# Kernel optimization log

Measured on AMD Instinct MI355X. Metric: run time of the kernel, lower is better.

## Reference

```python
import jax, jax.numpy as jnp
import numpy as np

N_NODES = 50000
N_EDGES = 1600000
D_IN = 128
D_OUT = 32
ALPHA = 0.2  # LeakyReLU negative slope


def setup_inputs() -> dict:
    key = jax.random.key(0)
    k1, k2, k3, k4, k5, k6 = jax.random.split(key, 6)
    gain = float(np.sqrt(2.0))  # relu gain, xavier_normal-style scale
    X = jax.random.normal(k1, (N_NODES, D_IN), dtype=jnp.float32)
    weights = jax.random.normal(k2, (D_IN, D_OUT), dtype=jnp.float32) * (gain * np.sqrt(2.0 / (D_IN + D_OUT)))
    a0 = jax.random.normal(k3, (1, D_OUT), dtype=jnp.float32) * (gain * np.sqrt(2.0 / (1 + D_OUT)))
    a1 = jax.random.normal(k4, (1, D_OUT), dtype=jnp.float32) * (gain * np.sqrt(2.0 / (1 + D_OUT)))
    row_idx = jax.random.randint(k5, (N_EDGES,), 0, N_NODES, dtype=jnp.int32)
    col_idx = jax.random.randint(k6, (N_EDGES,), 0, N_NODES, dtype=jnp.int32)
    return {"X": X, "weights": weights, "a0": a0, "a1": a1,
            "row_idx": row_idx, "col_idx": col_idx}


def _minmax_norm(v):
    vmin = jnp.min(v)
    vmax = jnp.max(v)
    return (v - vmin) / (vmax - vmin)


def reference(X, weights, a0, a1, row_idx, col_idx):
    # X_prime = X @ W  -> [N, D]
    X_prime = X @ weights
    # Per-node partial scores; edge score e(i->j) = a0.X_prime[i] + a1.X_prime[j]
    s0 = jnp.sum(X_prime * a0, axis=-1)  # [N]
    s1 = jnp.sum(X_prime * a1, axis=-1)  # [N]
    att = s0[row_idx] + s1[col_idx]      # [E]
    # leakyrelu -> min-max normalize over all edges -> exp
    att = jax.nn.leaky_relu(att, negative_slope=ALPHA)
    att = jnp.exp(_minmax_norm(att))
    # rows_sum = SpMM(att, ones) = per-destination-row sum of edge weights
    rows_sum = jax.ops.segment_sum(att, row_idx, num_segments=N_NODES)  # [N]
    # h_prime = SpMM(att, X_prime) / rows_sum  (dropout p=0 -> identity)
    h = jax.ops.segment_sum(att[:, None] * X_prime[col_idx], row_idx,
                            num_segments=N_NODES)  # [N, D]
    return h / rows_sum[:, None]
```

## Files before the change

kernel.cpp:

```cpp
#include <hip/hip_runtime.h>
#include <hip/hip_bf16.h>
#include <math.h>

#define N_NODES 50000
#define N_EDGES 1600000
#define D_IN 128
#define D_OUT 32
#define ALPHA 0.2f

#define NB   1021
#define NBP  1024
#define RPB  49
#define CAP  2048
#define PT   8
#define PBK  256
#define EB   (PT * PBK)
#define NPB  ((N_EDGES + EB - 1) / EB)
#define XNPB 32
#define NXB  ((N_NODES + XNPB - 1) / XNPB)
#define XLS  33

__device__ __forceinline__ int enc_f(float x) {
    int i = __float_as_int(x);
    return i >= 0 ? i : (i ^ 0x7fffffff);
}
__device__ __forceinline__ float dec_f(int k) {
    return __int_as_float(k >= 0 ? k : (k ^ 0x7fffffff));
}
__device__ __forceinline__ unsigned short f2bf(float x) {
    __hip_bfloat16 h = __float2bfloat16(x);
    return *(unsigned short*)&h;
}
__device__ __forceinline__ float bf2f(unsigned short u) {
    return __uint_as_float((unsigned)u << 16);
}

__global__ __launch_bounds__(256) void k_gemm(const float* __restrict__ X,
                                              const float* __restrict__ W,
                                              const float* __restrict__ a0,
                                              const float* __restrict__ a1,
                                              unsigned short* __restrict__ Xpb,
                                              float* __restrict__ s0,
                                              float* __restrict__ s1,
                                              int* __restrict__ minmax,
                                              int* __restrict__ gcount) {
    __shared__ float4 Wl4[1024];
    __shared__ float4 Xl4[XNPB * XLS];
    const int tid = threadIdx.x;
    if (blockIdx.x == 0) {
        if (tid == 0) {
            minmax[0] = 0x7fffffff;
            minmax[1] = (int)0x80000000;
        }
        for (int i = tid; i < NBP; i += 256) gcount[i] = 0;
    }
    const int node0 = blockIdx.x * XNPB;
    {
        const float4* W4 = (const float4*)W;
#pragma unroll
        for (int i = 0; i < 4; ++i) Wl4[tid + 256 * i] = W4[tid + 256 * i];
        const float4* X4 = (const float4*)X + (size_t)node0 * (D_IN / 4);
        const int lim = (min(XNPB, N_NODES - node0)) * (D_IN / 4);
#pragma unroll
        for (int i = 0; i < 4; ++i) {
            const int idx = tid + 256 * i;
            const float4 v = (idx < lim) ? X4[idx]
                                         : make_float4(0.f, 0.f, 0.f, 0.f);
            Xl4[(idx >> 5) * XLS + (idx & 31)] = v;
        }
    }
    __syncthreads();
    const int g = tid >> 3;
    const int l = tid & 7;
    const int node = node0 + g;
    const float4* xr = &Xl4[g * XLS];
    float ax = 0.f, ay = 0.f, az = 0.f, aw = 0.f;
#pragma unroll 4
    for (int kk = 0; kk < D_IN / 4; ++kk) {
        const float4 xv = xr[kk];
        const float4 w0 = Wl4[(4 * kk + 0) * 8 + l];
        const float4 w1 = Wl4[(4 * kk + 1) * 8 + l];
        const float4 w2 = Wl4[(4 * kk + 2) * 8 + l];
        const float4 w3 = Wl4[(4 * kk + 3) * 8 + l];
        ax += xv.x * w0.x + xv.y * w1.x + xv.z * w2.x + xv.w * w3.x;
        ay += xv.x * w0.y + xv.y * w1.y + xv.z * w2.y + xv.w * w3.y;
        az += xv.x * w0.z + xv.y * w1.z + xv.z * w2.z + xv.w * w3.z;
        aw += xv.x * w0.w + xv.y * w1.w + xv.z * w2.w + xv.w * w3.w;
    }
    if (node < N_NODES) {
        uint2 pk;
        pk.x = ((unsigned)f2bf(ay) << 16) | f2bf(ax);
        pk.y = ((unsigned)f2bf(aw) << 16) | f2bf(az);
        ((uint2*)Xpb)[(size_t)node * 8 + l] = pk;
        const float4 av0 = ((const float4*)a0)[l];
        const float4 av1 = ((const float4*)a1)[l];
        float v0 = ax * av0.x + ay * av0.y + az * av0.z + aw * av0.w;
        float v1 = ax * av1.x + ay * av1.y + az * av1.z + aw * av1.w;
#pragma unroll
        for (int m = 4; m >= 1; m >>= 1) {
            v0 += __shfl_xor(v0, m);
            v1 += __shfl_xor(v1, m);
        }
        if (l == 0) { s0[node] = v0; s1[node] = v1; }
    }
}

__global__ __launch_bounds__(256) void k_edge(const int* __restrict__ row,
                                              const int* __restrict__ col,
                                              const float* __restrict__ s0,
                                              const float* __restrict__ s1,
                                              int* __restrict__ minmax,
                                              int* __restrict__ gcount,
                                              uint2* __restrict__ gEdges) {
    __shared__ int hist[NBP];
    __shared__ int lcur[NBP];
    __shared__ int smn[4], smx[4];
    const int tid = threadIdx.x;
    for (int i = tid; i < NBP; i += PBK) hist[i] = 0;
    __syncthreads();
    const int base = blockIdx.x * EB;
    unsigned px[PT];
    float    fa[PT];
    int cnt = 0;
    int kmin = 0x7fffffff, kmax = 0x80000000;
    if (base + EB <= N_EDGES) {
#pragma unroll
        for (int i = 0; i < PT / 4; ++i) {
            const int4 r4 = ((const int4*)(row + base))[tid + i * PBK];
            const int4 c4 = ((const int4*)(col + base))[tid + i * PBK];
            const int rr[4] = {r4.x, r4.y, r4.z, r4.w};
            const int cc[4] = {c4.x, c4.y, c4.z, c4.w};
#pragma unroll
            for (int j = 0; j < 4; ++j) {
                const int r = rr[j];
                const int c = cc[j];
                float a = s0[r] + s1[c];
                a = a > 0.f ? a : ALPHA * a;
                const int k = enc_f(a);
                kmin = min(kmin, k);
                kmax = max(kmax, k);
                const unsigned b = (unsigned)r / RPB;
                const unsigned lr = (unsigned)r - b * RPB;
                px[cnt] = (b << 22) | (lr << 16) | (unsigned)c;
                fa[cnt] = a;
                ++cnt;
                atomicAdd(&hist[b], 1);
            }
        }
    } else {
#pragma unroll
        for (int i = 0; i < PT; ++i) {
            const int e = base + i * PBK + tid;
            if (e >= N_EDGES) break;
            const int r = row[e];
            const int c = col[e];
            float a = s0[r] + s1[c];
            a = a > 0.f ? a : ALPHA * a;
            const int k = enc_f(a);
            kmin = min(kmin, k);
            kmax = max(kmax, k);
            const unsigned b = (unsigned)r / RPB;
            const unsigned lr = (unsigned)r - b * RPB;
            px[cnt] = (b << 22) | (lr << 16) | (unsigned)c;
            fa[cnt] = a;
            ++cnt;
            atomicAdd(&hist[b], 1);
        }
    }
    __syncthreads();
    for (int i = tid; i < NBP; i += PBK) {
        const int h = hist[i];
        lcur[i] = h > 0 ? atomicAdd(&gcount[i], h) : 0;
    }
    __syncthreads();
    for (int j = 0; j < cnt; ++j) {
        const unsigned p = px[j];
        const unsigned b = p >> 22;
        const int pos = atomicAdd(&lcur[b], 1);
        if (pos < CAP)
            gEdges[(size_t)b * CAP + pos] =
                make_uint2(p & 0x3FFFFFu, (unsigned)__float_as_int(fa[j]));
    }
#pragma unroll
    for (int m = 32; m >= 1; m >>= 1) {
        kmin = min(kmin, __shfl_xor(kmin, m));
        kmax = max(kmax, __shfl_xor(kmax, m));
    }
    const int wave = tid >> 6;
    if ((tid & 63) == 0) { smn[wave] = kmin; smx[wave] = kmax; }
    __syncthreads();
    if (tid == 0) {
#pragma unroll
        for (int w = 1; w < 4; ++w) {
            kmin = min(kmin, smn[w]);
            kmax = max(kmax, smx[w]);
        }
        atomicMin(&minmax[0], kmin);
        atomicMax(&minmax[1], kmax);
    }
}

__global__ __launch_bounds__(512, 8) void k_bucket(const int* __restrict__ gcount,
                                                   const uint2* __restrict__ gEdges,
                                                   const unsigned short* __restrict__ Xpb,
                                                   const int* __restrict__ minmax,
                                                   float* __restrict__ out) {
    __shared__ unsigned short scol[CAP];
    __shared__ float swt[CAP];
    __shared__ int off[RPB + 1];
    __shared__ int cur[RPB];
    const int b = blockIdx.x;
    const int t = threadIdx.x;
    const float mn = dec_f(minmax[0]);
    const float mx = dec_f(minmax[1]);
    const float inv = 1.0f / (mx - mn);
    const int cnt = min(gcount[b], CAP);
    const uint2* eb = gEdges + (size_t)b * CAP;

    if (t < RPB) cur[t] = 0;
    __syncthreads();
    for (int i = t; i < cnt; i += 512) atomicAdd(&cur[eb[i].x >> 16], 1);
    __syncthreads();
    if (t == 0) {
        int run = 0;
#pragma unroll
        for (int r = 0; r < RPB; ++r) { off[r] = run; run += cur[r]; }
        off[RPB] = run;
    }
    __syncthreads();
    if (t < RPB) cur[t] = off[t];
    __syncthreads();
    for (int i = t; i < cnt; i += 512) {
        const uint2 e = eb[i];
        const int lr = (int)(e.x >> 16);
        const int p = atomicAdd(&cur[lr], 1);
        if (p < CAP) {
            scol[p] = (unsigned short)(e.x & 0xFFFFu);
            swt[p] = __expf((__int_as_float(e.y) - mn) * inv);
        }
    }
    __syncthreads();

    const int proc = t >> 4;
    const int d2 = t & 15;
    const unsigned* Xp32 = (const unsigned*)Xpb;
    for (int lr = proc; lr < RPB; lr += 32) {
        const int s = off[lr];
        const int e2 = off[lr + 1];
        float pa0 = 0.f, pa1 = 0.f, pa2 = 0.f, pa3 = 0.f;
        float pb0 = 0.f, pb1 = 0.f, pb2 = 0.f, pb3 = 0.f;
        float w0s = 0.f, w1s = 0.f, w2s = 0.f, w3s = 0.f;
        int i = s;
        for (; i + 3 < e2; i += 4) {
            const int c0 = scol[i];
            const int c1 = scol[i + 1];
            const int c2 = scol[i + 2];
            const int c3 = scol[i + 3];
            const float w0 = swt[i];
            const float w1 = swt[i + 1];
            const float w2 = swt[i + 2];
            const float w3 = swt[i + 3];
            const unsigned u0 = Xp32[(size_t)c0 * 16 + d2];
            const unsigned u1 = Xp32[(size_t)c1 * 16 + d2];
            const unsigned u2 = Xp32[(size_t)c2 * 16 + d2];
            const unsigned u3 = Xp32[(size_t)c3 * 16 + d2];
            pa0 += w0 * bf2f((unsigned short)(u0 & 0xFFFFu));
            pb0 += w0 * bf2f((unsigned short)(u0 >> 16));
            pa1 += w1 * bf2f((unsigned short)(u1 & 0xFFFFu));
            pb1 += w1 * bf2f((unsigned short)(u1 >> 16));
            pa2 += w2 * bf2f((unsigned short)(u2 & 0xFFFFu));
            pb2 += w2 * bf2f((unsigned short)(u2 >> 16));
            pa3 += w3 * bf2f((unsigned short)(u3 & 0xFFFFu));
            pb3 += w3 * bf2f((unsigned short)(u3 >> 16));
            w0s += w0; w1s += w1; w2s += w2; w3s += w3;
        }
        for (; i < e2; ++i) {
            const float w = swt[i];
            const unsigned u = Xp32[(size_t)scol[i] * 16 + d2];
            pa0 += w * bf2f((unsigned short)(u & 0xFFFFu));
            pb0 += w * bf2f((unsigned short)(u >> 16));
            w0s += w;
        }
        const int r = b * RPB + lr;
        if (r < N_NODES) {
            const float ws = w0s + w1s + w2s + w3s;
            float2 o;
            o.x = (pa0 + pa1 + pa2 + pa3) / ws;
            o.y = (pb0 + pb1 + pb2 + pb3) / ws;
            ((float2*)out)[(size_t)r * 16 + d2] = o;
        }
    }
}

extern "C" void kernel_launch(void* const* d_in, const int* in_sizes, int n_in,
                              void* d_out, int out_size, void* d_ws, size_t ws_size,
                              hipStream_t stream) {
    const float* X  = (const float*)d_in[0];
    const float* W  = (const float*)d_in[1];
    const float* a0 = (const float*)d_in[2];
    const float* a1 = (const float*)d_in[3];
    const int* row  = (const int*)d_in[4];
    const int* col  = (const int*)d_in[5];
    float* out = (float*)d_out;

    float* ws = (float*)d_ws;
    int*   minmax = (int*)ws;
    int*   gcount = (int*)(ws + 64);
    float* s0 = ws + 64 + 2048;
    float* s1 = s0 + 50048;
    unsigned short* Xpb = (unsigned short*)(s1 + 50048);
    uint2* gEdges = (uint2*)(s1 + 50048 + 800000);

    k_gemm<<<NXB, 256, 0, stream>>>(X, W, a0, a1, Xpb, s0, s1, minmax, gcount);
    k_edge<<<NPB, 256, 0, stream>>>(row, col, s0, s1, minmax, gcount, gEdges);
    k_bucket<<<NB, 512, 0, stream>>>(gcount, gEdges, Xpb, minmax, out);
}
```

Measured before the change: 158.4 us.

## Decouple score computation via W·a and overlap GEMM with edge binning

A new lightweight kernel folds the attention vectors into the weights first (W·a0, W·a1), so the per-node scores come from a single dot product against X and no longer depend on the full X@W GEMM. The bf16 X' GEMM then runs in the same launch as the edge scoring and binning pass, with blocks interleaved 2:1, so the compute-heavy and atomic-heavy work can overlap. Per-bucket global counters are padded to a 16-int stride to cut atomic contention on shared cache lines. The cost is reading X twice and changing the floating-point summation order of the scores.

Measured after the change: 156.6 us. Within noise of the previous version (-1.1%).

```diff
diff --git a/kernel.cpp b/kernel.cpp
--- a/kernel.cpp
+++ b/kernel.cpp
@@ -12,6 +12,7 @@
 #define NBP  1024
 #define RPB  49
 #define CAP  2048
+#define GST  16
 #define PT   8
 #define PBK  256
 #define EB   (PT * PBK)
@@ -19,6 +20,7 @@
 #define XNPB 32
 #define NXB  ((N_NODES + XNPB - 1) / XNPB)
 #define XLS  33
+#define SNPB 32
 
 __device__ __forceinline__ int enc_f(float x) {
     int i = __float_as_int(x);
@@ -35,67 +37,54 @@
     return __uint_as_float((unsigned)u << 16);
 }
 
-__global__ __launch_bounds__(256) void k_gemm(const float* __restrict__ X,
-                                              const float* __restrict__ W,
-                                              const float* __restrict__ a0,
-                                              const float* __restrict__ a1,
-                                              unsigned short* __restrict__ Xpb,
-                                              float* __restrict__ s0,
-                                              float* __restrict__ s1,
-                                              int* __restrict__ minmax,
-                                              int* __restrict__ gcount) {
-    __shared__ float4 Wl4[1024];
-    __shared__ float4 Xl4[XNPB * XLS];
+__global__ __launch_bounds__(256) void k_s(const float* __restrict__ X,
+                                           const float* __restrict__ W,
+                                           const float* __restrict__ a0,
+                                           const float* __restrict__ a1,
+                                           float* __restrict__ s0,
+                                           float* __restrict__ s1,
+                                           int* __restrict__ minmax,
+                                           int* __restrict__ gcount) {
+    __shared__ float wa0[D_IN], wa1[D_IN];
     const int tid = threadIdx.x;
     if (blockIdx.x == 0) {
         if (tid == 0) {
             minmax[0] = 0x7fffffff;
             minmax[1] = (int)0x80000000;
         }
-        for (int i = tid; i < NBP; i += 256) gcount[i] = 0;
-    }
-    const int node0 = blockIdx.x * XNPB;
+        int4* g4 = (int4*)gcount;
+        for (int i = tid; i < NBP * GST / 4; i += 256)
+            g4[i] = make_int4(0, 0, 0, 0);
+    }
     {
-        const float4* W4 = (const float4*)W;
-#pragma unroll
-        for (int i = 0; i < 4; ++i) Wl4[tid + 256 * i] = W4[tid + 256 * i];
-        const float4* X4 = (const float4*)X + (size_t)node0 * (D_IN / 4);
-        const int lim = (min(XNPB, N_NODES - node0)) * (D_IN / 4);
-#pragma unroll
-        for (int i = 0; i < 4; ++i) {
-            const int idx = tid + 256 * i;
-            const float4 v = (idx < lim) ? X4[idx]
-                                         : make_float4(0.f, 0.f, 0.f, 0.f);
-            Xl4[(idx >> 5) * XLS + (idx & 31)] = v;
-        }
-    }
-    __syncthreads();
-    const int g = tid >> 3;
+        const int k = tid & 127;
+        const float4* Wr = (const float4*)(W + k * D_OUT);
+        const float4* A = (const float4*)((tid < 128) ? a0 : a1);
+        float acc = 0.f;
+#pragma unroll
+        for (int j = 0; j < 8; ++j) {
+            const float4 w = Wr[j];
+            const float4 a = A[j];
+            acc += w.x * a.x + w.y * a.y + w.z * a.z + w.w * a.w;
+        }
+        if (tid < 128) wa0[k] = acc; else wa1[k] = acc;
+    }
+    __syncthreads();
+    const int node = blockIdx.x * SNPB + (tid >> 3);
     const int l = tid & 7;
-    const int node = node0 + g;
-    const float4* xr = &Xl4[g * XLS];
-    float ax = 0.f, ay = 0.f, az = 0.f, aw = 0.f;
-#pragma unroll 4
-    for (int kk = 0; kk < D_IN / 4; ++kk) {
-        const float4 xv = xr[kk];
-        const float4 w0 = Wl4[(4 * kk + 0) * 8 + l];
-        const float4 w1 = Wl4[(4 * kk + 1) * 8 + l];
-        const float4 w2 = Wl4[(4 * kk + 2) * 8 + l];
-        const float4 w3 = Wl4[(4 * kk + 3) * 8 + l];
-        ax += xv.x * w0.x + xv.y * w1.x + xv.z * w2.x + xv.w * w3.x;
-        ay += xv.x * w0.y + xv.y * w1.y + xv.z * w2.y + xv.w * w3.y;
-        az += xv.x * w0.z + xv.y * w1.z + xv.z * w2.z + xv.w * w3.z;
-        aw += xv.x * w0.w + xv.y * w1.w + xv.z * w2.w + xv.w * w3.w;
-    }
     if (node < N_NODES) {
-        uint2 pk;
-        pk.x = ((unsigned)f2bf(ay) << 16) | f2bf(ax);
-        pk.y = ((unsigned)f2bf(aw) << 16) | f2bf(az);
-        ((uint2*)Xpb)[(size_t)node * 8 + l] = pk;
-        const float4 av0 = ((const float4*)a0)[l];
-        const float4 av1 = ((const float4*)a1)[l];
-        float v0 = ax * av0.x + ay * av0.y + az * av0.z + aw * av0.w;
-        float v1 = ax * av1.x + ay * av1.y + az * av1.z + aw * av1.w;
+        const float4* xr = (const float4*)(X + (size_t)node * D_IN) + l * 4;
+        const float4* p4 = (const float4*)wa0 + l * 4;
+        const float4* q4 = (const float4*)wa1 + l * 4;
+        float v0 = 0.f, v1 = 0.f;
+#pragma unroll
+        for (int j = 0; j < 4; ++j) {
+            const float4 x = xr[j];
+            const float4 p = p4[j];
+            const float4 q = q4[j];
+            v0 += x.x * p.x + x.y * p.y + x.z * p.z + x.w * p.w;
+            v1 += x.x * q.x + x.y * q.y + x.z * q.z + x.w * q.w;
+        }
 #pragma unroll
         for (int m = 4; m >= 1; m >>= 1) {
             v0 += __shfl_xor(v0, m);
@@ -105,35 +94,108 @@
     }
 }
 
-__global__ __launch_bounds__(256) void k_edge(const int* __restrict__ row,
-                                              const int* __restrict__ col,
-                                              const float* __restrict__ s0,
-                                              const float* __restrict__ s1,
-                                              int* __restrict__ minmax,
-                                              int* __restrict__ gcount,
-                                              uint2* __restrict__ gEdges) {
-    __shared__ int hist[NBP];
-    __shared__ int lcur[NBP];
-    __shared__ int smn[4], smx[4];
+__global__ __launch_bounds__(256) void k_fused(const float* __restrict__ X,
+                                               const float* __restrict__ W,
+                                               const int* __restrict__ row,
+                                               const int* __restrict__ col,
+                                               const float* __restrict__ s0,
+                                               const float* __restrict__ s1,
+                                               unsigned short* __restrict__ Xpb,
+                                               int* __restrict__ minmax,
+                                               int* __restrict__ gcount,
+                                               uint2* __restrict__ gEdges) {
+    __shared__ char smem[33280] __attribute__((aligned(16)));
     const int tid = threadIdx.x;
-    for (int i = tid; i < NBP; i += PBK) hist[i] = 0;
-    __syncthreads();
-    const int base = blockIdx.x * EB;
-    unsigned px[PT];
-    float    fa[PT];
-    int cnt = 0;
-    int kmin = 0x7fffffff, kmax = 0x80000000;
-    if (base + EB <= N_EDGES) {
-#pragma unroll
-        for (int i = 0; i < PT / 4; ++i) {
-            const int4 r4 = ((const int4*)(row + base))[tid + i * PBK];
-            const int4 c4 = ((const int4*)(col + base))[tid + i * PBK];
-            const int rr[4] = {r4.x, r4.y, r4.z, r4.w};
-            const int cc[4] = {c4.x, c4.y, c4.z, c4.w};
-#pragma unroll
-            for (int j = 0; j < 4; ++j) {
-                const int r = rr[j];
-                const int c = cc[j];
+    const int bid = blockIdx.x;
+    if (bid % 3 != 0) {
+        const int gid = bid - bid / 3 - 1;
+        if (gid >= NXB) return;
+        float4* Wl4 = (float4*)smem;
+        float4* Xl4 = (float4*)(smem + 16384);
+        const int node0 = gid * XNPB;
+        {
+            const float4* W4 = (const float4*)W;
+#pragma unroll
+            for (int i = 0; i < 4; ++i) Wl4[tid + 256 * i] = W4[tid + 256 * i];
+            const float4* X4 = (const float4*)X + (size_t)node0 * (D_IN / 4);
+            const int lim = (min(XNPB, N_NODES - node0)) * (D_IN / 4);
+#pragma unroll
+            for (int i = 0; i < 4; ++i) {
+                const int idx = tid + 256 * i;
+                const float4 v = (idx < lim) ? X4[idx]
+                                             : make_float4(0.f, 0.f, 0.f, 0.f);
+                Xl4[(idx >> 5) * XLS + (idx & 31)] = v;
+            }
+        }
+        __syncthreads();
+        const int g = tid >> 3;
+        const int l = tid & 7;
+        const int node = node0 + g;
+        const float4* xr = &Xl4[g * XLS];
+        float ax = 0.f, ay = 0.f, az = 0.f, aw = 0.f;
+#pragma unroll 4
+        for (int kk = 0; kk < D_IN / 4; ++kk) {
+            const float4 xv = xr[kk];
+            const float4 w0 = Wl4[(4 * kk + 0) * 8 + l];
+            const float4 w1 = Wl4[(4 * kk + 1) * 8 + l];
+            const float4 w2 = Wl4[(4 * kk + 2) * 8 + l];
+            const float4 w3 = Wl4[(4 * kk + 3) * 8 + l];
+            ax += xv.x * w0.x + xv.y * w1.x + xv.z * w2.x + xv.w * w3.x;
+            ay += xv.x * w0.y + xv.y * w1.y + xv.z * w2.y + xv.w * w3.y;
+            az += xv.x * w0.z + xv.y * w1.z + xv.z * w2.z + xv.w * w3.z;
+            aw += xv.x * w0.w + xv.y * w1.w + xv.z * w2.w + xv.w * w3.w;
+        }
+        if (node < N_NODES) {
+            uint2 pk;
+            pk.x = ((unsigned)f2bf(ay) << 16) | f2bf(ax);
+            pk.y = ((unsigned)f2bf(aw) << 16) | f2bf(az);
+            ((uint2*)Xpb)[(size_t)node * 8 + l] = pk;
+        }
+    } else {
+        const int bb = bid / 3;
+        if (bb >= NPB) return;
+        int* hist = (int*)smem;
+        int* lcur = (int*)(smem + 4096);
+        int* smn  = (int*)(smem + 8192);
+        int* smx  = (int*)(smem + 8256);
+        for (int i = tid; i < NBP; i += PBK) hist[i] = 0;
+        __syncthreads();
+        const int base = bb * EB;
+        unsigned px[PT];
+        float    fa[PT];
+        int cnt = 0;
+        int kmin = 0x7fffffff, kmax = 0x80000000;
+        if (base + EB <= N_EDGES) {
+#pragma unroll
+            for (int i = 0; i < PT / 4; ++i) {
+                const int4 r4 = ((const int4*)(row + base))[tid + i * PBK];
+                const int4 c4 = ((const int4*)(col + base))[tid + i * PBK];
+                const int rr[4] = {r4.x, r4.y, r4.z, r4.w};
+                const int cc[4] = {c4.x, c4.y, c4.z, c4.w};
+#pragma unroll
+                for (int j = 0; j < 4; ++j) {
+                    const int r = rr[j];
+                    const int c = cc[j];
+                    float a = s0[r] + s1[c];
+                    a = a > 0.f ? a : ALPHA * a;
+                    const int k = enc_f(a);
+                    kmin = min(kmin, k);
+                    kmax = max(kmax, k);
+                    const unsigned b = (unsigned)r / RPB;
+                    const unsigned lr = (unsigned)r - b * RPB;
+                    px[cnt] = (b << 22) | (lr << 16) | (unsigned)c;
+                    fa[cnt] = a;
+                    ++cnt;
+                    atomicAdd(&hist[b], 1);
+                }
+            }
+        } else {
+#pragma unroll
+            for (int i = 0; i < PT; ++i) {
+                const int e = base + i * PBK + tid;
+                if (e >= N_EDGES) break;
+                const int r = row[e];
+                const int c = col[e];
                 float a = s0[r] + s1[c];
                 a = a > 0.f ? a : ALPHA * a;
                 const int k = enc_f(a);
@@ -147,56 +209,37 @@
                 atomicAdd(&hist[b], 1);
             }
         }
-    } else {
-#pragma unroll
-        for (int i = 0; i < PT; ++i) {
-            const int e = base + i * PBK + tid;
-            if (e >= N_EDGES) break;
-            const int r = row[e];
-            const int c = col[e];
-            float a = s0[r] + s1[c];
-            a = a > 0.f ? a : ALPHA * a;
-            const int k = enc_f(a);
-            kmin = min(kmin, k);
-            kmax = max(kmax, k);
-            const unsigned b = (unsigned)r / RPB;
-            const unsigned lr = (unsigned)r - b * RPB;
-            px[cnt] = (b << 22) | (lr << 16) | (unsigned)c;
-            fa[cnt] = a;
-            ++cnt;
-            atomicAdd(&hist[b], 1);
-        }
-    }
-    __syncthreads();
-    for (int i = tid; i < NBP; i += PBK) {
-        const int h = hist[i];
-        lcur[i] = h > 0 ? atomicAdd(&gcount[i], h) : 0;
-    }
-    __syncthreads();
-    for (int j = 0; j < cnt; ++j) {
-        const unsigned p = px[j];
-        const unsigned b = p >> 22;
-        const int pos = atomicAdd(&lcur[b], 1);
-        if (pos < CAP)
-            gEdges[(size_t)b * CAP + pos] =
-                make_uint2(p & 0x3FFFFFu, (unsigned)__float_as_int(fa[j]));
-    }
-#pragma unroll
-    for (int m = 32; m >= 1; m >>= 1) {
-        kmin = min(kmin, __shfl_xor(kmin, m));
-        kmax = max(kmax, __shfl_xor(kmax, m));
-    }
-    const int wave = tid >> 6;
-    if ((tid & 63) == 0) { smn[wave] = kmin; smx[wave] = kmax; }
-    __syncthreads();
-    if (tid == 0) {
-#pragma unroll
-        for (int w = 1; w < 4; ++w) {
-            kmin = min(kmin, smn[w]);
-            kmax = max(kmax, smx[w]);
-        }
-        atomicMin(&minmax[0], kmin);
-        atomicMax(&minmax[1], kmax);
+        __syncthreads();
+        for (int i = tid; i < NBP; i += PBK) {
+            const int h = hist[i];
+            lcur[i] = h > 0 ? atomicAdd(&gcount[i << 4], h) : 0;
+        }
+        __syncthreads();
+        for (int j = 0; j < cnt; ++j) {
+            const unsigned p = px[j];
+            const unsigned b = p >> 22;
+            const int pos = atomicAdd(&lcur[b], 1);
+            if (pos < CAP)
+                gEdges[(size_t)b * CAP + pos] =
+                    make_uint2(p & 0x3FFFFFu, (unsigned)__float_as_int(fa[j]));
+        }
+#pragma unroll
+        for (int m = 32; m >= 1; m >>= 1) {
+            kmin = min(kmin, __shfl_xor(kmin, m));
+            kmax = max(kmax, __shfl_xor(kmax, m));
+        }
+        const int wave = tid >> 6;
+        if ((tid & 63) == 0) { smn[wave] = kmin; smx[wave] = kmax; }
+        __syncthreads();
+        if (tid == 0) {
+#pragma unroll
+            for (int w = 1; w < 4; ++w) {
+                kmin = min(kmin, smn[w]);
+                kmax = max(kmax, smx[w]);
+            }
+            atomicMin(&minmax[0], kmin);
+            atomicMax(&minmax[1], kmax);
+        }
     }
 }
 
@@ -214,7 +257,7 @@
     const float mn = dec_f(minmax[0]);
     const float mx = dec_f(minmax[1]);
     const float inv = 1.0f / (mx - mn);
-    const int cnt = min(gcount[b], CAP);
+    const int cnt = min(gcount[b << 4], CAP);
     const uint2* eb = gEdges + (size_t)b * CAP;
 
     if (t < RPB) cur[t] = 0;
@@ -306,12 +349,14 @@
     float* ws = (float*)d_ws;
     int*   minmax = (int*)ws;
     int*   gcount = (int*)(ws + 64);
-    float* s0 = ws + 64 + 2048;
+    float* s0 = ws + 64 + NBP * GST;
     float* s1 = s0 + 50048;
     unsigned short* Xpb = (unsigned short*)(s1 + 50048);
     uint2* gEdges = (uint2*)(s1 + 50048 + 800000);
 
-    k_gemm<<<NXB, 256, 0, stream>>>(X, W, a0, a1, Xpb, s0, s1, minmax, gcount);
-    k_edge<<<NPB, 256, 0, stream>>>(row, col, s0, s1, minmax, gcount, gEdges);
+    k_s<<<(N_NODES + SNPB - 1) / SNPB, 256, 0, stream>>>(X, W, a0, a1, s0, s1,
+                                                         minmax, gcount);
+    k_fused<<<NXB + NPB + 1, 256, 0, stream>>>(X, W, row, col, s0, s1, Xpb,
+                                               minmax, gcount, gEdges);
     k_bucket<<<NB, 512, 0, stream>>>(gcount, gEdges, Xpb, minmax, out);
 }
```

## Replace LDS histogram binning with padded global atomics and per-block minmax partials

Applied to the files above, without the earlier changes.

The edge kernel drops its shared-memory histogram and two-pass local cursor scheme. Each edge now claims its slot with a direct global atomicAdd on a bucket counter padded to 16 ints (one per 64-byte line) and is written immediately. Blocks shrink to 4 edges per thread, and the global atomicMin/Max is replaced by per-block min/max partials. Every bucket block re-reduces those partials, trading 1.6M global atomics and some redundant reduction work for fewer barriers, smaller register state and higher occupancy.

Result: slower. 192.0 us (+21.2%).

```diff
diff --git a/kernel.cpp b/kernel.cpp
--- a/kernel.cpp
+++ b/kernel.cpp
@@ -12,10 +12,11 @@
 #define NBP  1024
 #define RPB  49
 #define CAP  2048
-#define PT   8
-#define PBK  256
-#define EB   (PT * PBK)
-#define NPB  ((N_EDGES + EB - 1) / EB)
+#define GST  16
+#define EPT  4
+#define EBK  256
+#define EB   (EPT * EBK)
+#define NEB  ((N_EDGES + EB - 1) / EB)
 #define XNPB 32
 #define NXB  ((N_NODES + XNPB - 1) / XNPB)
 #define XLS  33
@@ -42,17 +43,15 @@
                                               unsigned short* __restrict__ Xpb,
                                               float* __restrict__ s0,
                                               float* __restrict__ s1,
-                                              int* __restrict__ minmax,
                                               int* __restrict__ gcount) {
     __shared__ float4 Wl4[1024];
     __shared__ float4 Xl4[XNPB * XLS];
     const int tid = threadIdx.x;
     if (blockIdx.x == 0) {
-        if (tid == 0) {
-            minmax[0] = 0x7fffffff;
-            minmax[1] = (int)0x80000000;
-        }
-        for (int i = tid; i < NBP; i += 256) gcount[i] = 0;
+        int4* g4 = (int4*)gcount;
+#pragma unroll
+        for (int i = 0; i < NBP * GST / 4 / 256; ++i)
+            g4[tid + 256 * i] = make_int4(0, 0, 0, 0);
     }
     const int node0 = blockIdx.x * XNPB;
     {
@@ -109,77 +108,59 @@
                                               const int* __restrict__ col,
                                               const float* __restrict__ s0,
                                               const float* __restrict__ s1,
-                                              int* __restrict__ minmax,
                                               int* __restrict__ gcount,
+                                              int2* __restrict__ mm,
                                               uint2* __restrict__ gEdges) {
-    __shared__ int hist[NBP];
-    __shared__ int lcur[NBP];
     __shared__ int smn[4], smx[4];
     const int tid = threadIdx.x;
-    for (int i = tid; i < NBP; i += PBK) hist[i] = 0;
-    __syncthreads();
     const int base = blockIdx.x * EB;
-    unsigned px[PT];
-    float    fa[PT];
-    int cnt = 0;
     int kmin = 0x7fffffff, kmax = 0x80000000;
     if (base + EB <= N_EDGES) {
-#pragma unroll
-        for (int i = 0; i < PT / 4; ++i) {
-            const int4 r4 = ((const int4*)(row + base))[tid + i * PBK];
-            const int4 c4 = ((const int4*)(col + base))[tid + i * PBK];
-            const int rr[4] = {r4.x, r4.y, r4.z, r4.w};
-            const int cc[4] = {c4.x, c4.y, c4.z, c4.w};
-#pragma unroll
-            for (int j = 0; j < 4; ++j) {
-                const int r = rr[j];
-                const int c = cc[j];
-                float a = s0[r] + s1[c];
+        const int4 r4 = ((const int4*)(row + base))[tid];
+        const int4 c4 = ((const int4*)(col + base))[tid];
+        const int rr[4] = {r4.x, r4.y, r4.z, r4.w};
+        const int cc[4] = {c4.x, c4.y, c4.z, c4.w};
+        float sr[4], sc[4];
+#pragma unroll
+        for (int j = 0; j < 4; ++j) { sr[j] = s0[rr[j]]; sc[j] = s1[cc[j]]; }
+#pragma unroll
+        for (int j = 0; j < 4; ++j) {
+            float a = sr[j] + sc[j];
+            a = a > 0.f ? a : ALPHA * a;
+            const int k = enc_f(a);
+            kmin = min(kmin, k);
+            kmax = max(kmax, k);
+            const unsigned r = (unsigned)rr[j];
+            const unsigned b = r / RPB;
+            const unsigned lr = r - b * RPB;
+            const int pos = atomicAdd(&gcount[b << 4], 1);
+            if (pos < CAP)
+                gEdges[(size_t)b * CAP + pos] =
+                    make_uint2((lr << 16) | (unsigned)cc[j],
+                               (unsigned)__float_as_int(a));
+        }
+    } else {
+#pragma unroll
+        for (int j = 0; j < 4; ++j) {
+            const int e = base + j * EBK + tid;
+            if (e < N_EDGES) {
+                const int rv = row[e];
+                const int cv = col[e];
+                float a = s0[rv] + s1[cv];
                 a = a > 0.f ? a : ALPHA * a;
                 const int k = enc_f(a);
                 kmin = min(kmin, k);
                 kmax = max(kmax, k);
-                const unsigned b = (unsigned)r / RPB;
-                const unsigned lr = (unsigned)r - b * RPB;
-                px[cnt] = (b << 22) | (lr << 16) | (unsigned)c;
-                fa[cnt] = a;
-                ++cnt;
-                atomicAdd(&hist[b], 1);
+                const unsigned r = (unsigned)rv;
+                const unsigned b = r / RPB;
+                const unsigned lr = r - b * RPB;
+                const int pos = atomicAdd(&gcount[b << 4], 1);
+                if (pos < CAP)
+                    gEdges[(size_t)b * CAP + pos] =
+                        make_uint2((lr << 16) | (unsigned)cv,
+                                   (unsigned)__float_as_int(a));
             }
         }
-    } else {
-#pragma unroll
-        for (int i = 0; i < PT; ++i) {
-            const int e = base + i * PBK + tid;
-            if (e >= N_EDGES) break;
-            const int r = row[e];
-            const int c = col[e];
-            float a = s0[r] + s1[c];
-            a = a > 0.f ? a : ALPHA * a;
-            const int k = enc_f(a);
-            kmin = min(kmin, k);
-            kmax = max(kmax, k);
-            const unsigned b = (unsigned)r / RPB;
-            const unsigned lr = (unsigned)r - b * RPB;
-            px[cnt] = (b << 22) | (lr << 16) | (unsigned)c;
-            fa[cnt] = a;
-            ++cnt;
-            atomicAdd(&hist[b], 1);
-        }
-    }
-    __syncthreads();
-    for (int i = tid; i < NBP; i += PBK) {
-        const int h = hist[i];
-        lcur[i] = h > 0 ? atomicAdd(&gcount[i], h) : 0;
-    }
-    __syncthreads();
-    for (int j = 0; j < cnt; ++j) {
-        const unsigned p = px[j];
-        const unsigned b = p >> 22;
-        const int pos = atomicAdd(&lcur[b], 1);
-        if (pos < CAP)
-            gEdges[(size_t)b * CAP + pos] =
-                make_uint2(p & 0x3FFFFFu, (unsigned)__float_as_int(fa[j]));
     }
 #pragma unroll
     for (int m = 32; m >= 1; m >>= 1) {
@@ -195,30 +176,51 @@
             kmin = min(kmin, smn[w]);
             kmax = max(kmax, smx[w]);
         }
-        atomicMin(&minmax[0], kmin);
-        atomicMax(&minmax[1], kmax);
+        mm[blockIdx.x] = make_int2(kmin, kmax);
     }
 }
 
 __global__ __launch_bounds__(512, 8) void k_bucket(const int* __restrict__ gcount,
                                                    const uint2* __restrict__ gEdges,
                                                    const unsigned short* __restrict__ Xpb,
-                                                   const int* __restrict__ minmax,
+                                                   const int2* __restrict__ mm,
                                                    float* __restrict__ out) {
     __shared__ unsigned short scol[CAP];
     __shared__ float swt[CAP];
     __shared__ int off[RPB + 1];
     __shared__ int cur[RPB];
+    __shared__ int rmn[8], rmx[8];
+    __shared__ float s_mn, s_inv;
     const int b = blockIdx.x;
     const int t = threadIdx.x;
-    const float mn = dec_f(minmax[0]);
-    const float mx = dec_f(minmax[1]);
-    const float inv = 1.0f / (mx - mn);
-    const int cnt = min(gcount[b], CAP);
+    const int cnt = min(gcount[b << 4], CAP);
     const uint2* eb = gEdges + (size_t)b * CAP;
 
+    int kmn = 0x7fffffff, kmx = 0x80000000;
+    for (int i = t; i < NEB; i += 512) {
+        const int2 v = mm[i];
+        kmn = min(kmn, v.x);
+        kmx = max(kmx, v.y);
+    }
+#pragma unroll
+    for (int m = 32; m >= 1; m >>= 1) {
+        kmn = min(kmn, __shfl_xor(kmn, m));
+        kmx = max(kmx, __shfl_xor(kmx, m));
+    }
+    if ((t & 63) == 0) { rmn[t >> 6] = kmn; rmx[t >> 6] = kmx; }
     if (t < RPB) cur[t] = 0;
     __syncthreads();
+    if (t == 0) {
+#pragma unroll
+        for (int w = 1; w < 8; ++w) {
+            kmn = min(kmn, rmn[w]);
+            kmx = max(kmx, rmx[w]);
+        }
+        const float mn = dec_f(kmn);
+        const float mx = dec_f(kmx);
+        s_mn = mn;
+        s_inv = 1.0f / (mx - mn);
+    }
     for (int i = t; i < cnt; i += 512) atomicAdd(&cur[eb[i].x >> 16], 1);
     __syncthreads();
     if (t == 0) {
@@ -230,6 +232,8 @@
     __syncthreads();
     if (t < RPB) cur[t] = off[t];
     __syncthreads();
+    const float mn = s_mn;
+    const float inv = s_inv;
     for (int i = t; i < cnt; i += 512) {
         const uint2 e = eb[i];
         const int lr = (int)(e.x >> 16);
@@ -304,14 +308,14 @@
     float* out = (float*)d_out;
 
     float* ws = (float*)d_ws;
-    int*   minmax = (int*)ws;
-    int*   gcount = (int*)(ws + 64);
-    float* s0 = ws + 64 + 2048;
+    int*   gcount = (int*)ws + 64;
+    int2*  mm = (int2*)((int*)ws + 64 + NBP * GST);
+    float* s0 = ws + 64 + NBP * GST + 3200;
     float* s1 = s0 + 50048;
     unsigned short* Xpb = (unsigned short*)(s1 + 50048);
     uint2* gEdges = (uint2*)(s1 + 50048 + 800000);
 
-    k_gemm<<<NXB, 256, 0, stream>>>(X, W, a0, a1, Xpb, s0, s1, minmax, gcount);
-    k_edge<<<NPB, 256, 0, stream>>>(row, col, s0, s1, minmax, gcount, gEdges);
-    k_bucket<<<NB, 512, 0, stream>>>(gcount, gEdges, Xpb, minmax, out);
-}
+    k_gemm<<<NXB, 256, 0, stream>>>(X, W, a0, a1, Xpb, s0, s1, gcount);
+    k_edge<<<NEB, 256, 0, stream>>>(row, col, s0, s1, gcount, mm, gEdges);
+    k_bucket<<<NB, 512, 0, stream>>>(gcount, gEdges, Xpb, mm, out);
+}
```
